# Optimization experiments

Measured on AMD Instinct MI355X. Metric: run time of the kernel, lower is better.

The kernel has to match this reference:

```python
import jax, jax.numpy as jnp
import numpy as np

DIM = 1536
NHEADS = 12
HDIM = DIM // NHEADS  # 128
EPS = 1e-6
LOCAL_ATTN_SIZE = 3
SINK_SIZE = 1
MAX_ATTN = 32760 if LOCAL_ATTN_SIZE == -1 else LOCAL_ATTN_SIZE * 1560  # 4680


def _rms(x, g):
    # WanRMSNorm over last dim
    return x * jax.lax.rsqrt(jnp.mean(x * x, axis=-1, keepdims=True) + EPS) * g


def _rope(x, f, h, w, fr, fi, start_frame):
    # x: [b, s, n, d] with s == f*h*w; fr/fi: [1024, d//2] real/imag of complex rotations
    b, s, n, d = x.shape
    c = d // 2
    c0 = c - 2 * (c // 3)
    c1 = c // 3
    fc = jax.lax.complex(fr, fi)  # [1024, c]
    xr = x.reshape(b, s, n, c, 2)
    xc = jax.lax.complex(xr[..., 0], xr[..., 1])  # [b, s, n, c]
    ff = fc[start_frame:start_frame + f, :c0]      # [f, c0]
    fh = fc[:h, c0:c0 + c1]                        # [h, c1]
    fw = fc[:w, c0 + c1:c0 + 2 * c1]               # [w, c1]
    freqs_i = jnp.concatenate([
        jnp.broadcast_to(ff[:, None, None, :], (f, h, w, c0)),
        jnp.broadcast_to(fh[None, :, None, :], (f, h, w, c1)),
        jnp.broadcast_to(fw[None, None, :, :], (f, h, w, c1)),
    ], axis=-1).reshape(1, s, 1, c)
    y = xc * freqs_i
    return jnp.stack([y.real, y.imag], axis=-1).reshape(b, s, n, d)


def _attn(q, k, v):
    # plain SDPA (decode path of the module uses no mask on the gathered window)
    scale = 1.0 / np.sqrt(q.shape[-1]).astype(np.float32)
    logits = jnp.einsum('bqnd,bknd->bnqk', q, k) * scale
    p = jax.nn.softmax(logits, axis=-1)
    return jnp.einsum('bnqk,bknd->bqnd', p, v)


def _forward(x, cache_k, cache_v, freqs_real, freqs_imag,
             wq, bq, wk, bk, wv, bv, wo, bo, gq, gk,
             f_frames, height, width, current_start, global_end_index, local_end_index):
    b, s, _ = x.shape
    n, d = NHEADS, HDIM
    frame_seqlen = height * width
    start_frame = current_start // frame_seqlen

    q = _rms(x @ wq + bq, gq).reshape(b, s, n, d)
    k = _rms(x @ wk + bk, gk).reshape(b, s, n, d)
    v = (x @ wv + bv).reshape(b, s, n, d)

    rq = _rope(q, f_frames, height, width, freqs_real, freqs_imag, start_frame)
    rk = _rope(k, f_frames, height, width, freqs_real, freqs_imag, start_frame)

    current_end = current_start + s
    sink_tokens = SINK_SIZE * frame_seqlen
    kv_size = cache_k.shape[1]
    is_recompute = (current_end <= global_end_index) and (current_start > 0)

    kc, vc = cache_k, cache_v
    if LOCAL_ATTN_SIZE != -1 and current_end > global_end_index and s + local_end_index > kv_size:
        # evict oldest non-sink tokens, roll the rest toward the sink region
        num_evicted = s + local_end_index - kv_size
        num_rolled = local_end_index - num_evicted - sink_tokens
        src = slice(sink_tokens + num_evicted, sink_tokens + num_evicted + num_rolled)
        kc = kc.at[:, sink_tokens:sink_tokens + num_rolled].set(jax.lax.stop_gradient(cache_k[:, src]))
        vc = vc.at[:, sink_tokens:sink_tokens + num_rolled].set(jax.lax.stop_gradient(cache_v[:, src]))
        new_local_end = local_end_index + current_end - global_end_index - num_evicted
    else:
        new_local_end = local_end_index + current_end - global_end_index
    local_start = new_local_end - s
    write_start = max(local_start, sink_tokens) if is_recompute else local_start
    off = max(0, write_start - local_start)
    wl = max(0, new_local_end - write_start)
    if wl > 0:
        kc = kc.at[:, write_start:new_local_end].set(rk[:, off:off + wl])
        vc = vc.at[:, write_start:new_local_end].set(v[:, off:off + wl])

    if sink_tokens > 0:
        budget = MAX_ATTN - sink_tokens
        if budget > 0:
            lo = max(sink_tokens, new_local_end - budget)
            kcat = jnp.concatenate([kc[:, :sink_tokens], kc[:, lo:new_local_end]], axis=1)
            vcat = jnp.concatenate([vc[:, :sink_tokens], vc[:, lo:new_local_end]], axis=1)
        else:
            kcat, vcat = kc[:, :sink_tokens], vc[:, :sink_tokens]
        o = _attn(rq, kcat, vcat)
    else:
        ws = max(0, new_local_end - MAX_ATTN)
        o = _attn(rq, kc[:, ws:new_local_end], vc[:, ws:new_local_end])

    return o.reshape(b, s, DIM) @ wo + bo


def setup_inputs() -> dict:
    key = jax.random.key(0)
    ks = jax.random.split(key, 12)
    B, S, CACHE = 1, 1560, 4680
    sc = 0.02
    # RoPE tables as unit-magnitude complex rotations
    ang = jax.random.uniform(ks[0], (1024, HDIM // 2), jnp.float32, 0.0, 2.0 * np.pi)
    return {
        'x': jax.random.normal(ks[1], (B, S, DIM), jnp.float32),
        'cache_k': jax.random.normal(ks[2], (B, CACHE, NHEADS, HDIM), jnp.float32),
        'cache_v': jax.random.normal(ks[3], (B, CACHE, NHEADS, HDIM), jnp.float32),
        'freqs_real': jnp.cos(ang),
        'freqs_imag': jnp.sin(ang),
        'wq': jax.random.normal(ks[4], (DIM, DIM), jnp.float32) * sc,
        'bq': jnp.zeros((DIM,), jnp.float32),
        'wk': jax.random.normal(ks[5], (DIM, DIM), jnp.float32) * sc,
        'bk': jnp.zeros((DIM,), jnp.float32),
        'wv': jax.random.normal(ks[6], (DIM, DIM), jnp.float32) * sc,
        'bv': jnp.zeros((DIM,), jnp.float32),
        'wo': jax.random.normal(ks[7], (DIM, DIM), jnp.float32) * sc,
        'bo': jnp.zeros((DIM,), jnp.float32),
        'gq': jnp.ones((DIM,), jnp.float32),
        'gk': jnp.ones((DIM,), jnp.float32),
        'f_frames': 1,
        'height': 30,
        'width': 52,
        'current_start': 4680,
        'global_end_index': 4680,
        'local_end_index': 4680,
    }


def reference(x, cache_k, cache_v, freqs_real, freqs_imag,
              wq, bq, wk, bk, wv, bv, wo, bo, gq, gk,
              f_frames, height, width, current_start, global_end_index, local_end_index):
    return _forward(x, cache_k, cache_v, freqs_real, freqs_imag,
                    wq, bq, wk, bk, wv, bv, wo, bo, gq, gk,
                    f_frames, height, width, current_start, global_end_index, local_end_index)
```

## Files before the change

kernel.cpp:

```cpp
#include <hip/hip_runtime.h>
#include <cstdint>
#include <cstddef>

typedef unsigned int  u32;
typedef unsigned short u16;
typedef short s16x8 __attribute__((ext_vector_type(8)));
typedef float f32x4 __attribute__((ext_vector_type(4)));

#define DIM     1536
#define NH      12
#define HD      128
#define SEQ     1560
#define MPAD    1664
#define NKV     4680
#define NKPAD   4736
#define ROLL0   3120
#define NQK     4608
#define START_FRAME 3
#define NEGINF  -3.0e4f
#define NSPLIT  3
#define SPLITKC 1600

__device__ __forceinline__ u16 f2bf(float f){
  u32 u = __builtin_bit_cast(u32, f);
  u32 r = (u + 0x7fffu + ((u >> 16) & 1u)) >> 16;
  return (u16)r;
}

__global__ void k_zero_pads(u16* __restrict__ Kc, u16* __restrict__ VT,
                            u16* __restrict__ Qr, u16* __restrict__ Opad){
  int i = blockIdx.x * 256 + threadIdx.x;
  uint4 z = make_uint4(0u, 0u, 0u, 0u);
  if (i < 10752){
    int h = i / 896, r = i % 896;
    ((uint4*)(Kc + ((size_t)h * NKPAD + NKV) * 128))[r] = z;
  } else if (i < 21504){
    int j = i - 10752; int row = j / 7, c = j % 7;
    ((uint4*)(VT + (size_t)row * NKPAD + NKV))[c] = z;
  } else if (i < 41472){
    int j = i - 21504; int h = j / 1664, r = j % 1664;
    ((uint4*)(Qr + ((size_t)h * MPAD + SEQ) * 128))[r] = z;
  } else if (i < 61440){
    int r = i - 41472;
    ((uint4*)(Opad + (size_t)SEQ * DIM))[r] = z;
  }
}

__global__ void k_prep_x(const float* __restrict__ x, u16* __restrict__ xp){
  int i = blockIdx.x * 256 + threadIdx.x;
  const int n_src = SEQ * DIM / 8;
  u16 o[8] = {0,0,0,0,0,0,0,0};
  if (i < n_src){
    float4 a = ((const float4*)x)[2*i];
    float4 b = ((const float4*)x)[2*i + 1];
    o[0]=f2bf(a.x); o[1]=f2bf(a.y); o[2]=f2bf(a.z); o[3]=f2bf(a.w);
    o[4]=f2bf(b.x); o[5]=f2bf(b.y); o[6]=f2bf(b.z); o[7]=f2bf(b.w);
  }
  uint4 v = make_uint4((u32)o[0]|((u32)o[1]<<16), (u32)o[2]|((u32)o[3]<<16),
                       (u32)o[4]|((u32)o[5]<<16), (u32)o[6]|((u32)o[7]<<16));
  ((uint4*)xp)[i] = v;
}

__global__ void k_transpose_w(const float* __restrict__ wq, const float* __restrict__ wk,
                              const float* __restrict__ wv, const float* __restrict__ wo,
                              u16* __restrict__ WT){
  __shared__ u32 tile[64][65];
  int z = blockIdx.z;
  const float* w = (z==0)?wq:(z==1)?wk:(z==2)?wv:wo;
  u16* dst = WT + (size_t)z * DIM * DIM;
  int r0 = blockIdx.x * 64, c0 = blockIdx.y * 64;
  int t = threadIdx.x;
  int rr = t >> 4, cg = t & 15;
#pragma unroll
  for (int i = 0; i < 4; i++){
    int r = rr + i * 16;
    float4 v = *(const float4*)(w + (size_t)(r0 + r) * DIM + c0 + cg * 4);
    tile[r][cg*4+0] = f2bf(v.x); tile[r][cg*4+1] = f2bf(v.y);
    tile[r][cg*4+2] = f2bf(v.z); tile[r][cg*4+3] = f2bf(v.w);
  }
  __syncthreads();
  int c = t >> 2, rg = t & 3;
  u32 wds[8];
#pragma unroll
  for (int j = 0; j < 8; j++)
    wds[j] = (tile[rg*16 + 2*j][c] & 0xffffu) | (tile[rg*16 + 2*j + 1][c] << 16);
  u16* q = dst + (size_t)(c0 + c) * DIM + r0 + rg * 16;
  *(uint4*)q       = make_uint4(wds[0], wds[1], wds[2], wds[3]);
  *(uint4*)(q + 8) = make_uint4(wds[4], wds[5], wds[6], wds[7]);
}

#define LDK 40
__global__ __launch_bounds__(256) void k_gemm_qkv(
    const u16* __restrict__ A, const u16* __restrict__ B,
    const float* __restrict__ biasq, const float* __restrict__ biask, const float* __restrict__ biasv,
    float* __restrict__ Y, float* __restrict__ sumsq){
  __shared__ u16 As[128*LDK];
  __shared__ u16 Bs[128*LDK];
  int m0 = blockIdx.y * 128, n0 = blockIdx.x * 128;
  int t = threadIdx.x, w = t >> 6, lane = t & 63, quad = lane >> 4, lc = lane & 15;
  int wm = w & 1, wn = w >> 1;
  int sr = t >> 1, sh = (t & 1) * 16;
  f32x4 acc[4][4] = {};
  for (int kt = 0; kt < DIM/32; kt++){
    int k0 = kt * 32;
    __syncthreads();
    {
      const uint4* ga = (const uint4*)(A + (size_t)(m0 + sr) * DIM + k0 + sh);
      uint4 a0 = ga[0], a1 = ga[1];
      const uint4* gb = (const uint4*)(B + (size_t)(n0 + sr) * DIM + k0 + sh);
      uint4 b0 = gb[0], b1 = gb[1];
      *(uint4*)(As + sr * LDK + sh)     = a0;
      *(uint4*)(As + sr * LDK + sh + 8) = a1;
      *(uint4*)(Bs + sr * LDK + sh)     = b0;
      *(uint4*)(Bs + sr * LDK + sh + 8) = b1;
    }
    __syncthreads();
    s16x8 af[4], bf[4];
#pragma unroll
    for (int mt = 0; mt < 4; mt++) af[mt] = *(const s16x8*)(As + (wm*64 + mt*16 + lc) * LDK + quad * 8);
#pragma unroll
    for (int nt = 0; nt < 4; nt++) bf[nt] = *(const s16x8*)(Bs + (wn*64 + nt*16 + lc) * LDK + quad * 8);
#pragma unroll
    for (int mt = 0; mt < 4; mt++)
#pragma unroll
      for (int nt = 0; nt < 4; nt++)
        acc[mt][nt] = __builtin_amdgcn_mfma_f32_16x16x32_bf16(af[mt], bf[nt], acc[mt][nt], 0, 0, 0);
  }
  const float* bias; int cbase; int which;
  if (n0 < DIM)        { bias = biasq; cbase = 0;     which = 0; }
  else if (n0 < 2*DIM) { bias = biask; cbase = DIM;   which = 1; }
  else                 { bias = biasv; cbase = 2*DIM; which = 2; }
  float bvals[4];
#pragma unroll
  for (int nt = 0; nt < 4; nt++) bvals[nt] = bias[n0 - cbase + wn*64 + nt*16 + lc];
#pragma unroll
  for (int mt = 0; mt < 4; mt++){
    int row0 = m0 + wm*64 + mt*16 + quad*4;
    float ss[4] = {0.f, 0.f, 0.f, 0.f};
#pragma unroll
    for (int nt = 0; nt < 4; nt++){
      int col = n0 + wn*64 + nt*16 + lc;
#pragma unroll
      for (int r = 0; r < 4; r++){
        float y = acc[mt][nt][r] + bvals[nt];
        Y[(size_t)(row0 + r) * NQK + col] = y;
        ss[r] += y * y;
      }
    }
    if (which < 2){
      float* dst = sumsq + (which ? MPAD : 0);
#pragma unroll
      for (int r = 0; r < 4; r++){
        float v = ss[r];
        v += __shfl_xor(v, 1); v += __shfl_xor(v, 2); v += __shfl_xor(v, 4); v += __shfl_xor(v, 8);
        if (lc == 0) atomicAdd(&dst[row0 + r], v);
      }
    }
  }
}

__global__ void k_rope_qk(const float* __restrict__ Y, const float* __restrict__ sumsq,
                          const float* __restrict__ gq, const float* __restrict__ gk,
                          const float* __restrict__ fre, const float* __restrict__ fim,
                          u16* __restrict__ Qr, u16* __restrict__ Kc){
  int pos = blockIdx.x;
  int t = threadIdx.x;
  float scq = rsqrtf(sumsq[pos]        * (1.0f/1536.0f) + 1e-6f);
  float sck = rsqrtf(sumsq[MPAD + pos] * (1.0f/1536.0f) + 1e-6f);
  int hrow = pos / 52, wrow = pos % 52;
#pragma unroll
  for (int i = 0; i < 3; i++){
    int p = t + i * 256;
    int head = p >> 6, j = p & 63;
    int frow = (j < 22) ? START_FRAME : ((j < 43) ? hrow : wrow);
    float cr = fre[frow * 64 + j], ci = fim[frow * 64 + j];
    int d0 = head * 128 + 2 * j;
    float2 yq = *(const float2*)(Y + (size_t)pos * NQK + d0);
    float qa = yq.x * scq * gq[d0];
    float qb = yq.y * scq * gq[d0 + 1];
    u32 oq = (u32)f2bf(qa * cr - qb * ci) | ((u32)f2bf(qa * ci + qb * cr) << 16);
    *(u32*)(Qr + (size_t)(head * MPAD + pos) * 128 + 2 * j) = oq;
    float2 yk = *(const float2*)(Y + (size_t)pos * NQK + DIM + d0);
    float ka = yk.x * sck * gk[d0];
    float kb = yk.y * sck * gk[d0 + 1];
    u32 ok = (u32)f2bf(ka * cr - kb * ci) | ((u32)f2bf(ka * ci + kb * cr) << 16);
    *(u32*)(Kc + (size_t)(head * NKPAD + ROLL0 + pos) * 128 + 2 * j) = ok;
  }
}

__global__ void k_copy_cache_k(const float* __restrict__ ck, u16* __restrict__ Kc){
  int p = blockIdx.x;
  int src = (p < SEQ) ? p : p + SEQ;
  int t = threadIdx.x;
  int h = t >> 4, d = (t & 15) * 8;
  const float* s = ck + (size_t)src * DIM + t * 8;
  float4 a = ((const float4*)s)[0], b = ((const float4*)s)[1];
  uint4 v = make_uint4((u32)f2bf(a.x)|((u32)f2bf(a.y)<<16), (u32)f2bf(a.z)|((u32)f2bf(a.w)<<16),
                       (u32)f2bf(b.x)|((u32)f2bf(b.y)<<16), (u32)f2bf(b.z)|((u32)f2bf(b.w)<<16));
  *(uint4*)(Kc + (size_t)(h * NKPAD + p) * 128 + d) = v;
}

__global__ void k_tv_cache(const float* __restrict__ cv, u16* __restrict__ VT){
  __shared__ u32 tile[64][65];
  int p0 = blockIdx.x * 64, hd0 = blockIdx.y * 64;
  int t = threadIdx.x;
  int pr = t >> 4, cg = t & 15;
#pragma unroll
  for (int i = 0; i < 4; i++){
    int p = p0 + pr + i * 16;
    if (p < ROLL0){
      int src = (p < SEQ) ? p : p + SEQ;
      float4 v = *(const float4*)(cv + (size_t)src * DIM + hd0 + cg * 4);
      tile[pr + i*16][cg*4+0] = f2bf(v.x); tile[pr + i*16][cg*4+1] = f2bf(v.y);
      tile[pr + i*16][cg*4+2] = f2bf(v.z); tile[pr + i*16][cg*4+3] = f2bf(v.w);
    }
  }
  __syncthreads();
  int hd = t >> 2, pg = t & 3;
  int pbase = p0 + pg * 16;
  if (pbase < ROLL0){
    u32 wds[8];
#pragma unroll
    for (int j = 0; j < 8; j++)
      wds[j] = (tile[pg*16 + 2*j][hd] & 0xffffu) | (tile[pg*16 + 2*j + 1][hd] << 16);
    u16* q = VT + (size_t)(hd0 + hd) * NKPAD + pbase;
    *(uint4*)q       = make_uint4(wds[0], wds[1], wds[2], wds[3]);
    *(uint4*)(q + 8) = make_uint4(wds[4], wds[5], wds[6], wds[7]);
  }
}

__global__ void k_tv_new(const float* __restrict__ Y, u16* __restrict__ VT){
  __shared__ u32 tile[64][65];
  int p0 = blockIdx.x * 64, hd0 = blockIdx.y * 64;
  int t = threadIdx.x;
  int pr = t >> 4, cg = t & 15;
#pragma unroll
  for (int i = 0; i < 4; i++){
    int p = p0 + pr + i * 16;
    if (p < SEQ){
      float4 v = *(const float4*)(Y + (size_t)p * NQK + 2*DIM + hd0 + cg * 4);
      tile[pr + i*16][cg*4+0] = f2bf(v.x); tile[pr + i*16][cg*4+1] = f2bf(v.y);
      tile[pr + i*16][cg*4+2] = f2bf(v.z); tile[pr + i*16][cg*4+3] = f2bf(v.w);
    }
  }
  __syncthreads();
  int hd = t >> 2, pg = t & 3;
  int pbase = p0 + pg * 16;
  u32 wds[8];
#pragma unroll
  for (int j = 0; j < 8; j++)
    wds[j] = (tile[pg*16 + 2*j][hd] & 0xffffu) | (tile[pg*16 + 2*j + 1][hd] << 16);
  u16* q = VT + (size_t)(hd0 + hd) * NKPAD + ROLL0 + pbase;
  if (pbase + 8  <= SEQ) *(uint4*)q       = make_uint4(wds[0], wds[1], wds[2], wds[3]);
  if (pbase + 16 <= SEQ) *(uint4*)(q + 8) = make_uint4(wds[4], wds[5], wds[6], wds[7]);
}

#define LDKS 136
#define LDVS 72
__global__ __launch_bounds__(512, 4) void k_attn(const u16* __restrict__ Qr, const u16* __restrict__ Kc,
                                                 const u16* __restrict__ VT,
                                                 float* __restrict__ Opart, float* __restrict__ ml){
  __shared__ u16 Ks[64 * LDKS];
  __shared__ u16 Vs[128 * LDVS];
  __shared__ u16 Ps[8][16 * LDVS];
  int h = blockIdx.y, qb = blockIdx.x, sp = blockIdx.z;
  int t = threadIdx.x, w = t >> 6, lane = t & 63, quad = lane >> 4, lc = lane & 15;
  int qbase = qb * 128 + w * 16;
  const u16* Qbase = Qr + (size_t)(h * MPAD + qbase + lc) * 128;
  s16x8 qf[4];
#pragma unroll
  for (int kk = 0; kk < 4; kk++) qf[kk] = *(const s16x8*)(Qbase + kk * 32 + quad * 8);
  f32x4 oacc[8] = {};
  float m_[4] = {NEGINF, NEGINF, NEGINF, NEGINF};
  float l_[4] = {0.f, 0.f, 0.f, 0.f};
  const float scale = 0.08838834764831845f;
  const u16* Kh = Kc + (size_t)h * NKPAD * 128;
  const u16* Vh = VT + (size_t)h * 128 * NKPAD;
  u16* Pw = &Ps[w][0];
  int kr0 = t >> 4,          kg0 = (t & 15) * 8;
  int kr1 = (t + 512) >> 4,  kg1 = ((t + 512) & 15) * 8;
  int vd0 = t >> 3,          vp0 = (t & 7) * 8;
  int vd1 = (t + 512) >> 3,  vp1 = ((t + 512) & 7) * 8;

  int kc0 = sp * SPLITKC;
  int kc1 = (sp == NSPLIT-1) ? NKPAD : kc0 + SPLITKC;
  uint4 kp0, kp1, vp0r, vp1r;
  {
    int kc = kc0;
    kp0  = *(const uint4*)(Kh + (size_t)(kc + kr0) * 128 + kg0);
    kp1  = *(const uint4*)(Kh + (size_t)(kc + kr1) * 128 + kg1);
    vp0r = *(const uint4*)(Vh + (size_t)vd0 * NKPAD + kc + vp0);
    vp1r = *(const uint4*)(Vh + (size_t)vd1 * NKPAD + kc + vp1);
  }
  for (int kc = kc0; kc < kc1; kc += 64){
    __syncthreads();
    *(uint4*)(Ks + kr0 * LDKS + kg0) = kp0;
    *(uint4*)(Ks + kr1 * LDKS + kg1) = kp1;
    *(uint4*)(Vs + vd0 * LDVS + vp0) = vp0r;
    *(uint4*)(Vs + vd1 * LDVS + vp1) = vp1r;
    __syncthreads();
    if (kc + 64 < kc1){
      int kn = kc + 64;
      kp0  = *(const uint4*)(Kh + (size_t)(kn + kr0) * 128 + kg0);
      kp1  = *(const uint4*)(Kh + (size_t)(kn + kr1) * 128 + kg1);
      vp0r = *(const uint4*)(Vh + (size_t)vd0 * NKPAD + kn + vp0);
      vp1r = *(const uint4*)(Vh + (size_t)vd1 * NKPAD + kn + vp1);
    }
    float s[4][4];
#pragma unroll
    for (int nt = 0; nt < 4; nt++){
      f32x4 acc = {};
      int p = nt * 16 + lc;
#pragma unroll
      for (int kk = 0; kk < 4; kk++){
        s16x8 bfr = *(const s16x8*)(Ks + p * LDKS + (kk * 4 + quad) * 8);
        acc = __builtin_amdgcn_mfma_f32_16x16x32_bf16(qf[kk], bfr, acc, 0, 0, 0);
      }
#pragma unroll
      for (int r = 0; r < 4; r++) s[nt][r] = acc[r] * scale;
    }
    if (kc + 64 > NKV){
#pragma unroll
      for (int nt = 0; nt < 4; nt++){
        int col = kc + nt * 16 + lc;
        if (col >= NKV){
#pragma unroll
          for (int r = 0; r < 4; r++) s[nt][r] = NEGINF;
        }
      }
    }
    float mn[4], alpha[4];
#pragma unroll
    for (int r = 0; r < 4; r++){
      float mx = fmaxf(fmaxf(s[0][r], s[1][r]), fmaxf(s[2][r], s[3][r]));
      mx = fmaxf(mx, __shfl_xor(mx, 1)); mx = fmaxf(mx, __shfl_xor(mx, 2));
      mx = fmaxf(mx, __shfl_xor(mx, 4)); mx = fmaxf(mx, __shfl_xor(mx, 8));
      mn[r] = fmaxf(m_[r], mx);
      alpha[r] = __expf(m_[r] - mn[r]);
      m_[r] = mn[r];
    }
#pragma unroll
    for (int nt = 0; nt < 4; nt++)
#pragma unroll
      for (int r = 0; r < 4; r++) s[nt][r] = __expf(s[nt][r] - mn[r]);
#pragma unroll
    for (int r = 0; r < 4; r++){
      float sum = s[0][r] + s[1][r] + s[2][r] + s[3][r];
      sum += __shfl_xor(sum, 1); sum += __shfl_xor(sum, 2);
      sum += __shfl_xor(sum, 4); sum += __shfl_xor(sum, 8);
      l_[r] = l_[r] * alpha[r] + sum;
    }
#pragma unroll
    for (int dt = 0; dt < 8; dt++){
      f32x4 oo = oacc[dt];
#pragma unroll
      for (int r = 0; r < 4; r++) oo[r] *= alpha[r];
      oacc[dt] = oo;
    }
#pragma unroll
    for (int nt = 0; nt < 4; nt++)
#pragma unroll
      for (int r = 0; r < 4; r++){
        int row = quad * 4 + r;
        Pw[row * LDVS + nt * 16 + lc] = f2bf(s[nt][r]);
      }
    asm volatile("s_waitcnt lgkmcnt(0)" ::: "memory");
    s16x8 a0 = *(const s16x8*)(Pw + lc * LDVS + quad * 8);
    s16x8 a1 = *(const s16x8*)(Pw + lc * LDVS + 32 + quad * 8);
#pragma unroll
    for (int dt = 0; dt < 8; dt++){
      int d = dt * 16 + lc;
      s16x8 v0 = *(const s16x8*)(Vs + d * LDVS + quad * 8);
      s16x8 v1 = *(const s16x8*)(Vs + d * LDVS + 32 + quad * 8);
      oacc[dt] = __builtin_amdgcn_mfma_f32_16x16x32_bf16(a0, v0, oacc[dt], 0, 0, 0);
      oacc[dt] = __builtin_amdgcn_mfma_f32_16x16x32_bf16(a1, v1, oacc[dt], 0, 0, 0);
    }
  }
  float* Ob = Opart + ((size_t)(sp * NH + h) * MPAD) * 128;
  float* mlb = ml + ((size_t)(sp * NH + h) * MPAD) * 2;
#pragma unroll
  for (int dt = 0; dt < 8; dt++)
#pragma unroll
    for (int r = 0; r < 4; r++){
      int row = qbase + quad * 4 + r;
      Ob[(size_t)row * 128 + dt * 16 + lc] = oacc[dt][r];
    }
  if (lc == 0){
#pragma unroll
    for (int r = 0; r < 4; r++){
      int row = qbase + quad * 4 + r;
      mlb[row * 2 + 0] = m_[r];
      mlb[row * 2 + 1] = l_[r];
    }
  }
}

__global__ void k_attn_cmb(const float* __restrict__ Opart, const float* __restrict__ ml,
                           u16* __restrict__ Og){
  int row = blockIdx.x, h = blockIdx.y, d = threadIdx.x;
  float m0 = ml[((size_t)(0 * NH + h) * MPAD + row) * 2 + 0];
  float l0 = ml[((size_t)(0 * NH + h) * MPAD + row) * 2 + 1];
  float m1 = ml[((size_t)(1 * NH + h) * MPAD + row) * 2 + 0];
  float l1 = ml[((size_t)(1 * NH + h) * MPAD + row) * 2 + 1];
  float m2 = ml[((size_t)(2 * NH + h) * MPAD + row) * 2 + 0];
  float l2 = ml[((size_t)(2 * NH + h) * MPAD + row) * 2 + 1];
  float M = fmaxf(fmaxf(m0, m1), m2);
  float w0 = __expf(m0 - M), w1 = __expf(m1 - M), w2 = __expf(m2 - M);
  float L = w0 * l0 + w1 * l1 + w2 * l2;
  float o0 = Opart[((size_t)(0 * NH + h) * MPAD + row) * 128 + d];
  float o1 = Opart[((size_t)(1 * NH + h) * MPAD + row) * 128 + d];
  float o2 = Opart[((size_t)(2 * NH + h) * MPAD + row) * 128 + d];
  float o = (w0 * o0 + w1 * o1 + w2 * o2) / L;
  Og[(size_t)row * DIM + h * 128 + d] = f2bf(o);
}

__global__ __launch_bounds__(256) void k_gemm_out(const u16* __restrict__ A, const u16* __restrict__ B,
                                                  const float* __restrict__ bo, float* __restrict__ out){
  __shared__ u16 As[128*LDK];
  __shared__ u16 Bs[128*LDK];
  int m0 = blockIdx.y * 128, n0 = blockIdx.x * 128;
  int t = threadIdx.x, w = t >> 6, lane = t & 63, quad = lane >> 4, lc = lane & 15;
  int wm = w & 1, wn = w >> 1;
  int sr = t >> 1, sh = (t & 1) * 16;
  f32x4 acc[4][4] = {};
  for (int kt = 0; kt < DIM/32; kt++){
    int k0 = kt * 32;
    __syncthreads();
    {
      const uint4* ga = (const uint4*)(A + (size_t)(m0 + sr) * DIM + k0 + sh);
      uint4 a0 = ga[0], a1 = ga[1];
      const uint4* gb = (const uint4*)(B + (size_t)(n0 + sr) * DIM + k0 + sh);
      uint4 b0 = gb[0], b1 = gb[1];
      *(uint4*)(As + sr * LDK + sh)     = a0;
      *(uint4*)(As + sr * LDK + sh + 8) = a1;
      *(uint4*)(Bs + sr * LDK + sh)     = b0;
      *(uint4*)(Bs + sr * LDK + sh + 8) = b1;
    }
    __syncthreads();
    s16x8 af[4], bf[4];
#pragma unroll
    for (int mt = 0; mt < 4; mt++) af[mt] = *(const s16x8*)(As + (wm*64 + mt*16 + lc) * LDK + quad * 8);
#pragma unroll
    for (int nt = 0; nt < 4; nt++) bf[nt] = *(const s16x8*)(Bs + (wn*64 + nt*16 + lc) * LDK + quad * 8);
#pragma unroll
    for (int mt = 0; mt < 4; mt++)
#pragma unroll
      for (int nt = 0; nt < 4; nt++)
        acc[mt][nt] = __builtin_amdgcn_mfma_f32_16x16x32_bf16(af[mt], bf[nt], acc[mt][nt], 0, 0, 0);
  }
  float bvals[4];
#pragma unroll
  for (int nt = 0; nt < 4; nt++) bvals[nt] = bo[n0 + wn*64 + nt*16 + lc];
#pragma unroll
  for (int mt = 0; mt < 4; mt++){
    int row0 = m0 + wm*64 + mt*16 + quad*4;
#pragma unroll
    for (int nt = 0; nt < 4; nt++){
      int col = n0 + wn*64 + nt*16 + lc;
#pragma unroll
      for (int r = 0; r < 4; r++){
        int row = row0 + r;
        if (row < SEQ) out[(size_t)row * DIM + col] = acc[mt][nt][r] + bvals[nt];
      }
    }
  }
}

extern "C" void kernel_launch(void* const* d_in, const int* in_sizes, int n_in,
                              void* d_out, int out_size, void* d_ws, size_t ws_size,
                              hipStream_t stream){
  const float* x   = (const float*)d_in[0];
  const float* ck  = (const float*)d_in[1];
  const float* cv  = (const float*)d_in[2];
  const float* fre = (const float*)d_in[3];
  const float* fim = (const float*)d_in[4];
  const float* wq  = (const float*)d_in[5];
  const float* bq  = (const float*)d_in[6];
  const float* wk  = (const float*)d_in[7];
  const float* bk  = (const float*)d_in[8];
  const float* wv  = (const float*)d_in[9];
  const float* bv  = (const float*)d_in[10];
  const float* wo  = (const float*)d_in[11];
  const float* bo  = (const float*)d_in[12];
  const float* gq  = (const float*)d_in[13];
  const float* gk  = (const float*)d_in[14];

  char* ws = (char*)d_ws;
  size_t off = 0;
  u16*   xpad  = (u16*)(ws + off);  off += (size_t)MPAD * DIM * 2;
  u16*   WT    = (u16*)(ws + off);  off += (size_t)4 * DIM * DIM * 2;
  float* Y     = (float*)(ws + off); off += (size_t)MPAD * NQK * 4;
  float* sumsq = (float*)(ws + off); off += (size_t)2 * MPAD * 4;
  u16*   Qr    = (u16*)(ws + off);  off += (size_t)NH * MPAD * 128 * 2;
  u16*   Kc    = (u16*)(ws + off);  off += (size_t)NH * NKPAD * 128 * 2;
  u16*   VT    = (u16*)(ws + off);  off += (size_t)NH * 128 * NKPAD * 2;
  u16*   Opad  = (u16*)(ws + off);  off += (size_t)MPAD * DIM * 2;
  if (off > ws_size) return;
  float* Opart = Y;
  float* ml    = (float*)xpad;

  hipMemsetAsync(sumsq, 0, (size_t)2 * MPAD * 4, stream);
  k_zero_pads   <<<dim3(240), 256, 0, stream>>>(Kc, VT, Qr, Opad);
  k_prep_x      <<<dim3(MPAD*DIM/8/256), 256, 0, stream>>>(x, xpad);
  k_transpose_w <<<dim3(24, 24, 4), 256, 0, stream>>>(wq, wk, wv, wo, WT);
  k_gemm_qkv    <<<dim3(NQK/128, MPAD/128), 256, 0, stream>>>(xpad, WT, bq, bk, bv, Y, sumsq);
  k_rope_qk     <<<dim3(SEQ), 256, 0, stream>>>(Y, sumsq, gq, gk, fre, fim, Qr, Kc);
  k_copy_cache_k<<<dim3(ROLL0), 192, 0, stream>>>(ck, Kc);
  k_tv_cache    <<<dim3(49, 24), 256, 0, stream>>>(cv, VT);
  k_tv_new      <<<dim3(25, 24), 256, 0, stream>>>(Y, VT);
  k_attn        <<<dim3(MPAD/128, NH, NSPLIT), 512, 0, stream>>>(Qr, Kc, VT, Opart, ml);
  k_attn_cmb    <<<dim3(SEQ, NH), 128, 0, stream>>>(Opart, ml, Opad);
  k_gemm_out    <<<dim3(DIM/128, MPAD/128), 256, 0, stream>>>(Opad, WT + (size_t)3*DIM*DIM, bo, (float*)d_out);
}
```

Measured before the change: 395.9 us.

## Increase attention KV splits, defer softmax rescale, fuse prep kernels, use exp2

Raises the attention KV split count from 3 to 5 so more blocks fill the GPU, and makes the combine kernel generic over the split count. The online softmax now skips rescaling the accumulator unless a row max grows past a threshold, and it uses exp2 with the log2e factor folded into the scale. It also adds MFMA priority hints, changes the LDS padding for V and P, and merges the zero-pad, memset and x-conversion work into one launch. The workspace is rearranged so the larger partial-output buffers fit, with the wo weights moved out of the region that is overwritten. The risks are extra partial-output traffic in the combine step and possible overflow from deferred rescaling if a logit rises more than the threshold above the stored max.

```diff
diff --git a/kernel.cpp b/kernel.cpp
--- a/kernel.cpp
+++ b/kernel.cpp
@@ -18,8 +18,10 @@
 #define NQK     4608
 #define START_FRAME 3
 #define NEGINF  -3.0e4f
-#define NSPLIT  3
-#define SPLITKC 1600
+#define NSPLIT  5
+#define SPLITKC 960
+
+#define EXP2F(x) exp2f(x)
 
 __device__ __forceinline__ u16 f2bf(float f){
   u32 u = __builtin_bit_cast(u32, f);
@@ -27,47 +29,52 @@
   return (u16)r;
 }
 
-__global__ void k_zero_pads(u16* __restrict__ Kc, u16* __restrict__ VT,
-                            u16* __restrict__ Qr, u16* __restrict__ Opad){
-  int i = blockIdx.x * 256 + threadIdx.x;
-  uint4 z = make_uint4(0u, 0u, 0u, 0u);
-  if (i < 10752){
-    int h = i / 896, r = i % 896;
-    ((uint4*)(Kc + ((size_t)h * NKPAD + NKV) * 128))[r] = z;
-  } else if (i < 21504){
-    int j = i - 10752; int row = j / 7, c = j % 7;
-    ((uint4*)(VT + (size_t)row * NKPAD + NKV))[c] = z;
-  } else if (i < 41472){
-    int j = i - 21504; int h = j / 1664, r = j % 1664;
-    ((uint4*)(Qr + ((size_t)h * MPAD + SEQ) * 128))[r] = z;
-  } else if (i < 61440){
-    int r = i - 41472;
-    ((uint4*)(Opad + (size_t)SEQ * DIM))[r] = z;
-  }
-}
-
-__global__ void k_prep_x(const float* __restrict__ x, u16* __restrict__ xp){
-  int i = blockIdx.x * 256 + threadIdx.x;
-  const int n_src = SEQ * DIM / 8;
-  u16 o[8] = {0,0,0,0,0,0,0,0};
-  if (i < n_src){
-    float4 a = ((const float4*)x)[2*i];
-    float4 b = ((const float4*)x)[2*i + 1];
-    o[0]=f2bf(a.x); o[1]=f2bf(a.y); o[2]=f2bf(a.z); o[3]=f2bf(a.w);
-    o[4]=f2bf(b.x); o[5]=f2bf(b.y); o[6]=f2bf(b.z); o[7]=f2bf(b.w);
-  }
-  uint4 v = make_uint4((u32)o[0]|((u32)o[1]<<16), (u32)o[2]|((u32)o[3]<<16),
-                       (u32)o[4]|((u32)o[5]<<16), (u32)o[6]|((u32)o[7]<<16));
-  ((uint4*)xp)[i] = v;
+__global__ void k_pre(const float* __restrict__ x, u16* __restrict__ xp,
+                      u16* __restrict__ Kc, u16* __restrict__ VT,
+                      u16* __restrict__ Qr, u16* __restrict__ Opad,
+                      float* __restrict__ sumsq){
+  int b = blockIdx.x;
+  if (b < 244){
+    int i = b * 256 + threadIdx.x;
+    uint4 z = make_uint4(0u, 0u, 0u, 0u);
+    if (i < 10752){
+      int h = i / 896, r = i % 896;
+      ((uint4*)(Kc + ((size_t)h * NKPAD + NKV) * 128))[r] = z;
+    } else if (i < 21504){
+      int j = i - 10752; int row = j / 7, c = j % 7;
+      ((uint4*)(VT + (size_t)row * NKPAD + NKV))[c] = z;
+    } else if (i < 41472){
+      int j = i - 21504; int h = j / 1664, r = j % 1664;
+      ((uint4*)(Qr + ((size_t)h * MPAD + SEQ) * 128))[r] = z;
+    } else if (i < 61440){
+      int r = i - 41472;
+      ((uint4*)(Opad + (size_t)SEQ * DIM))[r] = z;
+    } else if (i < 62272){
+      ((uint4*)sumsq)[i - 61440] = z;
+    }
+  } else {
+    int i = (b - 244) * 256 + threadIdx.x;
+    const int n_src = SEQ * DIM / 8;
+    u16 o[8] = {0,0,0,0,0,0,0,0};
+    if (i < n_src){
+      float4 a = ((const float4*)x)[2*i];
+      float4 c = ((const float4*)x)[2*i + 1];
+      o[0]=f2bf(a.x); o[1]=f2bf(a.y); o[2]=f2bf(a.z); o[3]=f2bf(a.w);
+      o[4]=f2bf(c.x); o[5]=f2bf(c.y); o[6]=f2bf(c.z); o[7]=f2bf(c.w);
+    }
+    uint4 v = make_uint4((u32)o[0]|((u32)o[1]<<16), (u32)o[2]|((u32)o[3]<<16),
+                         (u32)o[4]|((u32)o[5]<<16), (u32)o[6]|((u32)o[7]<<16));
+    ((uint4*)xp)[i] = v;
+  }
 }
 
 __global__ void k_transpose_w(const float* __restrict__ wq, const float* __restrict__ wk,
                               const float* __restrict__ wv, const float* __restrict__ wo,
-                              u16* __restrict__ WT){
+                              u16* __restrict__ WTqkv, u16* __restrict__ WTo){
   __shared__ u32 tile[64][65];
   int z = blockIdx.z;
   const float* w = (z==0)?wq:(z==1)?wk:(z==2)?wv:wo;
-  u16* dst = WT + (size_t)z * DIM * DIM;
+  u16* dst = (z < 3) ? (WTqkv + (size_t)z * DIM * DIM) : WTo;
   int r0 = blockIdx.x * 64, c0 = blockIdx.y * 64;
   int t = threadIdx.x;
   int rr = t >> 4, cg = t & 15;
@@ -256,13 +263,15 @@
 }
 
 #define LDKS 136
-#define LDVS 72
+#define LDVS 68
+#define LDPS 76
+#define DEFER_THR 12.0f
 __global__ __launch_bounds__(512, 4) void k_attn(const u16* __restrict__ Qr, const u16* __restrict__ Kc,
                                                  const u16* __restrict__ VT,
                                                  float* __restrict__ Opart, float* __restrict__ ml){
   __shared__ u16 Ks[64 * LDKS];
   __shared__ u16 Vs[128 * LDVS];
-  __shared__ u16 Ps[8][16 * LDVS];
+  __shared__ u16 Ps[8][16 * LDPS];
   int h = blockIdx.y, qb = blockIdx.x, sp = blockIdx.z;
   int t = threadIdx.x, w = t >> 6, lane = t & 63, quad = lane >> 4, lc = lane & 15;
   int qbase = qb * 128 + w * 16;
@@ -273,7 +282,7 @@
   f32x4 oacc[8] = {};
   float m_[4] = {NEGINF, NEGINF, NEGINF, NEGINF};
   float l_[4] = {0.f, 0.f, 0.f, 0.f};
-  const float scale = 0.08838834764831845f;
+  const float scale = 0.08838834764831845f * 1.4426950408889634f;
   const u16* Kh = Kc + (size_t)h * NKPAD * 128;
   const u16* Vh = VT + (size_t)h * 128 * NKPAD;
   u16* Pw = &Ps[w][0];
@@ -307,6 +316,7 @@
       vp1r = *(const uint4*)(Vh + (size_t)vd1 * NKPAD + kn + vp1);
     }
     float s[4][4];
+    __builtin_amdgcn_s_setprio(1);
 #pragma unroll
     for (int nt = 0; nt < 4; nt++){
       f32x4 acc = {};
@@ -319,6 +329,7 @@
 #pragma unroll
       for (int r = 0; r < 4; r++) s[nt][r] = acc[r] * scale;
     }
+    __builtin_amdgcn_s_setprio(0);
     if (kc + 64 > NKV){
 #pragma unroll
       for (int nt = 0; nt < 4; nt++){
@@ -329,44 +340,55 @@
         }
       }
     }
-    float mn[4], alpha[4];
+    float mx_[4];
+    bool grow = false;
 #pragma unroll
     for (int r = 0; r < 4; r++){
       float mx = fmaxf(fmaxf(s[0][r], s[1][r]), fmaxf(s[2][r], s[3][r]));
       mx = fmaxf(mx, __shfl_xor(mx, 1)); mx = fmaxf(mx, __shfl_xor(mx, 2));
       mx = fmaxf(mx, __shfl_xor(mx, 4)); mx = fmaxf(mx, __shfl_xor(mx, 8));
-      mn[r] = fmaxf(m_[r], mx);
-      alpha[r] = __expf(m_[r] - mn[r]);
-      m_[r] = mn[r];
+      mx_[r] = mx;
+      grow = grow || (mx > m_[r] + DEFER_THR);
+    }
+    if (__any((int)grow)){
+      float alpha[4];
+#pragma unroll
+      for (int r = 0; r < 4; r++){
+        float mnew = fmaxf(m_[r], mx_[r]);
+        alpha[r] = EXP2F(m_[r] - mnew);
+        m_[r] = mnew;
+        l_[r] *= alpha[r];
+      }
+#pragma unroll
+      for (int dt = 0; dt < 8; dt++){
+        f32x4 oo = oacc[dt];
+#pragma unroll
+        for (int r = 0; r < 4; r++) oo[r] *= alpha[r];
+        oacc[dt] = oo;
+      }
     }
 #pragma unroll
     for (int nt = 0; nt < 4; nt++)
 #pragma unroll
-      for (int r = 0; r < 4; r++) s[nt][r] = __expf(s[nt][r] - mn[r]);
+      for (int r = 0; r < 4; r++) s[nt][r] = EXP2F(s[nt][r] - m_[r]);
 #pragma unroll
     for (int r = 0; r < 4; r++){
       float sum = s[0][r] + s[1][r] + s[2][r] + s[3][r];
       sum += __shfl_xor(sum, 1); sum += __shfl_xor(sum, 2);
       sum += __shfl_xor(sum, 4); sum += __shfl_xor(sum, 8);
-      l_[r] = l_[r] * alpha[r] + sum;
-    }
-#pragma unroll
-    for (int dt = 0; dt < 8; dt++){
-      f32x4 oo = oacc[dt];
-#pragma unroll
-      for (int r = 0; r < 4; r++) oo[r] *= alpha[r];
-      oacc[dt] = oo;
+      l_[r] += sum;
     }
 #pragma unroll
     for (int nt = 0; nt < 4; nt++)
 #pragma unroll
       for (int r = 0; r < 4; r++){
         int row = quad * 4 + r;
-        Pw[row * LDVS + nt * 16 + lc] = f2bf(s[nt][r]);
+        Pw[row * LDPS + nt * 16 + lc] = f2bf(s[nt][r]);
       }
     asm volatile("s_waitcnt lgkmcnt(0)" ::: "memory");
-    s16x8 a0 = *(const s16x8*)(Pw + lc * LDVS + quad * 8);
-    s16x8 a1 = *(const s16x8*)(Pw + lc * LDVS + 32 + quad * 8);
+    s16x8 a0 = *(const s16x8*)(Pw + lc * LDPS + quad * 8);
+    s16x8 a1 = *(const s16x8*)(Pw + lc * LDPS + 32 + quad * 8);
+    __builtin_amdgcn_s_setprio(1);
 #pragma unroll
     for (int dt = 0; dt < 8; dt++){
       int d = dt * 16 + lc;
@@ -375,22 +397,25 @@
       oacc[dt] = __builtin_amdgcn_mfma_f32_16x16x32_bf16(a0, v0, oacc[dt], 0, 0, 0);
       oacc[dt] = __builtin_amdgcn_mfma_f32_16x16x32_bf16(a1, v1, oacc[dt], 0, 0, 0);
     }
-  }
-  float* Ob = Opart + ((size_t)(sp * NH + h) * MPAD) * 128;
-  float* mlb = ml + ((size_t)(sp * NH + h) * MPAD) * 2;
+    __builtin_amdgcn_s_setprio(0);
+  }
+  float* Ob = Opart + ((size_t)(sp * NH + h) * SEQ) * 128;
+  float* mlb = ml + ((size_t)(sp * NH + h) * SEQ) * 2;
 #pragma unroll
   for (int dt = 0; dt < 8; dt++)
 #pragma unroll
     for (int r = 0; r < 4; r++){
       int row = qbase + quad * 4 + r;
-      Ob[(size_t)row * 128 + dt * 16 + lc] = oacc[dt][r];
+      if (row < SEQ) Ob[(size_t)row * 128 + dt * 16 + lc] = oacc[dt][r];
     }
   if (lc == 0){
 #pragma unroll
     for (int r = 0; r < 4; r++){
       int row = qbase + quad * 4 + r;
-      mlb[row * 2 + 0] = m_[r];
-      mlb[row * 2 + 1] = l_[r];
+      if (row < SEQ){
+        mlb[row * 2 + 0] = m_[r];
+        mlb[row * 2 + 1] = l_[r];
+      }
     }
   }
 }
@@ -398,20 +423,22 @@
 __global__ void k_attn_cmb(const float* __restrict__ Opart, const float* __restrict__ ml,
                            u16* __restrict__ Og){
   int row = blockIdx.x, h = blockIdx.y, d = threadIdx.x;
-  float m0 = ml[((size_t)(0 * NH + h) * MPAD + row) * 2 + 0];
-  float l0 = ml[((size_t)(0 * NH + h) * MPAD + row) * 2 + 1];
-  float m1 = ml[((size_t)(1 * NH + h) * MPAD + row) * 2 + 0];
-  float l1 = ml[((size_t)(1 * NH + h) * MPAD + row) * 2 + 1];
-  float m2 = ml[((size_t)(2 * NH + h) * MPAD + row) * 2 + 0];
-  float l2 = ml[((size_t)(2 * NH + h) * MPAD + row) * 2 + 1];
-  float M = fmaxf(fmaxf(m0, m1), m2);
-  float w0 = __expf(m0 - M), w1 = __expf(m1 - M), w2 = __expf(m2 - M);
-  float L = w0 * l0 + w1 * l1 + w2 * l2;
-  float o0 = Opart[((size_t)(0 * NH + h) * MPAD + row) * 128 + d];
-  float o1 = Opart[((size_t)(1 * NH + h) * MPAD + row) * 128 + d];
-  float o2 = Opart[((size_t)(2 * NH + h) * MPAD + row) * 128 + d];
-  float o = (w0 * o0 + w1 * o1 + w2 * o2) / L;
-  Og[(size_t)row * DIM + h * 128 + d] = f2bf(o);
+  float m[NSPLIT], l[NSPLIT];
+  float M = NEGINF;
+#pragma unroll
+  for (int s = 0; s < NSPLIT; s++){
+    m[s] = ml[((size_t)(s * NH + h) * SEQ + row) * 2 + 0];
+    l[s] = ml[((size_t)(s * NH + h) * SEQ + row) * 2 + 1];
+    M = fmaxf(M, m[s]);
+  }
+  float L = 0.f, o = 0.f;
+#pragma unroll
+  for (int s = 0; s < NSPLIT; s++){
+    float wgt = EXP2F(m[s] - M);
+    L += wgt * l[s];
+    o += wgt * Opart[((size_t)(s * NH + h) * SEQ + row) * 128 + d];
+  }
+  Og[(size_t)row * DIM + h * 128 + d] = f2bf(o / L);
 }
 
 __global__ __launch_bounds__(256) void k_gemm_out(const u16* __restrict__ A, const u16* __restrict__ B,
@@ -488,27 +515,26 @@
   char* ws = (char*)d_ws;
   size_t off = 0;
   u16*   xpad  = (u16*)(ws + off);  off += (size_t)MPAD * DIM * 2;
-  u16*   WT    = (u16*)(ws + off);  off += (size_t)4 * DIM * DIM * 2;
+  u16*   WTqkv = (u16*)(ws + off);  off += (size_t)3 * DIM * DIM * 2;
   float* Y     = (float*)(ws + off); off += (size_t)MPAD * NQK * 4;
+  u16*   WTo   = (u16*)(ws + off);  off += (size_t)DIM * DIM * 2;
   float* sumsq = (float*)(ws + off); off += (size_t)2 * MPAD * 4;
   u16*   Qr    = (u16*)(ws + off);  off += (size_t)NH * MPAD * 128 * 2;
   u16*   Kc    = (u16*)(ws + off);  off += (size_t)NH * NKPAD * 128 * 2;
   u16*   VT    = (u16*)(ws + off);  off += (size_t)NH * 128 * NKPAD * 2;
   u16*   Opad  = (u16*)(ws + off);  off += (size_t)MPAD * DIM * 2;
   if (off > ws_size) return;
-  float* Opart = Y;
-  float* ml    = (float*)xpad;
-
-  hipMemsetAsync(sumsq, 0, (size_t)2 * MPAD * 4, stream);
-  k_zero_pads   <<<dim3(240), 256, 0, stream>>>(Kc, VT, Qr, Opad);
-  k_prep_x      <<<dim3(MPAD*DIM/8/256), 256, 0, stream>>>(x, xpad);
-  k_transpose_w <<<dim3(24, 24, 4), 256, 0, stream>>>(wq, wk, wv, wo, WT);
-  k_gemm_qkv    <<<dim3(NQK/128, MPAD/128), 256, 0, stream>>>(xpad, WT, bq, bk, bv, Y, sumsq);
+  float* Opart = (float*)ws;
+  float* ml    = (float*)(ws + (size_t)NSPLIT * NH * SEQ * 128 * 4);
+
+  k_pre         <<<dim3(1492), 256, 0, stream>>>(x, xpad, Kc, VT, Qr, Opad, sumsq);
+  k_transpose_w <<<dim3(24, 24, 4), 256, 0, stream>>>(wq, wk, wv, wo, WTqkv, WTo);
+  k_gemm_qkv    <<<dim3(NQK/128, MPAD/128), 256, 0, stream>>>(xpad, WTqkv, bq, bk, bv, Y, sumsq);
   k_rope_qk     <<<dim3(SEQ), 256, 0, stream>>>(Y, sumsq, gq, gk, fre, fim, Qr, Kc);
   k_copy_cache_k<<<dim3(ROLL0), 192, 0, stream>>>(ck, Kc);
   k_tv_cache    <<<dim3(49, 24), 256, 0, stream>>>(cv, VT);
   k_tv_new      <<<dim3(25, 24), 256, 0, stream>>>(Y, VT);
   k_attn        <<<dim3(MPAD/128, NH, NSPLIT), 512, 0, stream>>>(Qr, Kc, VT, Opart, ml);
   k_attn_cmb    <<<dim3(SEQ, NH), 128, 0, stream>>>(Opart, ml, Opad);
-  k_gemm_out    <<<dim3(DIM/128, MPAD/128), 256, 0, stream>>>(Opad, WT + (size_t)3*DIM*DIM, bo, (float*)d_out);
-}
+  k_gemm_out    <<<dim3(DIM/128, MPAD/128), 256, 0, stream>>>(Opad, WTo, bo, (float*)d_out);
+}
```

After: 439.7 us. +11.1%, slower.
